# Optimization experiments

Measured on AMD Instinct MI355X. Metric: run time of the kernel, lower is better.

## Reference

```python
import jax, jax.numpy as jnp
import numpy as np

B, H, T, DK = 4, 8, 2048, 64

def setup_inputs() -> dict:
    key = jax.random.key(0)
    kq, kk, kv, kb = jax.random.split(key, 4)
    return {
        "Q": jax.random.normal(kq, (B, H, T, DK), dtype=jnp.float32),
        "K": jax.random.normal(kk, (B, H, T, DK), dtype=jnp.float32),
        "V": jax.random.normal(kv, (B, H, T, DK), dtype=jnp.float32),
        "attn_bias": jax.random.normal(kb, (H, T, T), dtype=jnp.float32),
    }

def reference(Q, K, V, attn_bias):
    # scores = Q K^T / sqrt(d_k) + bias  (bias added post-scaling, as in source)
    d_k = Q.shape[-1]
    scale = 1.0 / jnp.sqrt(jnp.asarray(d_k, Q.dtype))
    scores = jnp.einsum("bhqd,bhkd->bhqk", Q, K) * scale + attn_bias
    attn_weights = jax.nn.softmax(scores, axis=-1)  # (B,H,T,T), rows sum to 1
    # Dropout is identity in eval/reference mode; output uses (pre-dropout) weights.
    output = jnp.einsum("bhqk,bhkd->bhqd", attn_weights, V)
    return (output, attn_weights)
```

## Files before the change

kernel.cpp:

```cpp
#include <hip/hip_runtime.h>
#include <hip/hip_bf16.h>

#define TT   2048
#define DKK  64
#define NHH  8
#define NBB  4
#define QB   128
#define KBLK 64
#define NKT  (TT / KBLK)
#define NJ1  (NKT / 2)
#define LDE  72
#define TILE (KBLK * LDE)
#define SCALE 0.125f

#define SOFT_BARRIER() do {                                         \
    asm volatile("s_waitcnt lgkmcnt(0)" ::: "memory");              \
    __builtin_amdgcn_s_barrier();                                   \
    asm volatile("" ::: "memory");                                  \
} while (0)

typedef __attribute__((ext_vector_type(4))) float  f32x4;
typedef __attribute__((ext_vector_type(8))) __bf16 bf16x8;
typedef __attribute__((ext_vector_type(4))) __bf16 bf16x4;

__global__ __launch_bounds__(256)
void cast_k_kernel(const float* __restrict__ K, __bf16* __restrict__ Kb) {
    size_t i = ((size_t)blockIdx.x * 256 + threadIdx.x) * 8;
    f32x4 a = *(const f32x4*)(K + i);
    f32x4 b = *(const f32x4*)(K + i + 4);
    bf16x8 o = {(__bf16)a[0], (__bf16)a[1], (__bf16)a[2], (__bf16)a[3],
                (__bf16)b[0], (__bf16)b[1], (__bf16)b[2], (__bf16)b[3]};
    *(bf16x8*)(Kb + i) = o;
}

__global__ __launch_bounds__(256)
void vt_kernel(const float* __restrict__ V, __bf16* __restrict__ Vt) {
    __shared__ __bf16 tile[DKK][72];
    const int bh = blockIdx.y;
    const int t0 = blockIdx.x * 64;
    const int tid = threadIdx.x;
    const float* Vb = V + ((size_t)bh * TT + t0) * DKK;
    #pragma unroll
    for (int i = 0; i < 4; ++i) {
        int idx = tid + i * 256;
        int row = idx >> 4, c4 = idx & 15;
        f32x4 v = *(const f32x4*)(Vb + row * DKK + c4 * 4);
        tile[c4 * 4 + 0][row] = (__bf16)v[0];
        tile[c4 * 4 + 1][row] = (__bf16)v[1];
        tile[c4 * 4 + 2][row] = (__bf16)v[2];
        tile[c4 * 4 + 3][row] = (__bf16)v[3];
    }
    __syncthreads();
    __bf16* out = Vt + (size_t)bh * DKK * TT + t0;
    #pragma unroll
    for (int i = 0; i < 2; ++i) {
        int idx = tid + i * 256;
        int d = idx >> 3, ch = idx & 7;
        bf16x8 o = *(const bf16x8*)&tile[d][ch * 8];
        *(bf16x8*)(out + (size_t)d * TT + ch * 8) = o;
    }
}

__global__ __launch_bounds__(512, 4)
void sdpa_main(const float* __restrict__ Qp, const float* __restrict__ Bp,
               const __bf16* __restrict__ Kb, const __bf16* __restrict__ Vt,
               float* __restrict__ Op, float* __restrict__ Wp)
{
    __shared__ __bf16 Bl[4][TILE];
    __shared__ __bf16 Pl[8][16 * LDE];

    const int tid  = threadIdx.x;
    const int lane = tid & 63;
    const int w    = tid >> 6;
    const int g    = lane >> 4;
    const int ql   = lane & 15;

    const int id  = blockIdx.x;
    const int h   = id & 7;
    const int r   = id >> 3;
    const int qt  = r & 15;
    const int b   = r >> 4;
    const int bh  = b * NHH + h;

    const int q_local = w * 16 + ql;
    const int q_glob  = qt * QB + q_local;

    const __bf16* Kbh = Kb + (size_t)bh * TT * DKK;
    const __bf16* Vbh = Vt + (size_t)bh * DKK * TT;
    const float* biasRow = Bp + ((size_t)h * TT + q_glob) * TT;

    const int srow = tid >> 3;
    const int sch  = tid & 7;

    const float* qrow = Qp + ((size_t)bh * TT + q_glob) * DKK;
    f32x4 qa = *(const f32x4*)(qrow + g * 8);
    f32x4 qc = *(const f32x4*)(qrow + g * 8 + 4);
    f32x4 qe = *(const f32x4*)(qrow + 32 + g * 8);
    f32x4 qf = *(const f32x4*)(qrow + 32 + g * 8 + 4);
    const bf16x8 qfrag0 = {(__bf16)qa[0], (__bf16)qa[1], (__bf16)qa[2], (__bf16)qa[3],
                           (__bf16)qc[0], (__bf16)qc[1], (__bf16)qc[2], (__bf16)qc[3]};
    const bf16x8 qfrag1 = {(__bf16)qe[0], (__bf16)qe[1], (__bf16)qe[2], (__bf16)qe[3],
                           (__bf16)qf[0], (__bf16)qf[1], (__bf16)qf[2], (__bf16)qf[3]};

    #pragma unroll
    for (int t = 0; t < 2; ++t) {
        *(bf16x8*)&Bl[t][srow * LDE + sch * 8] =
            *(const bf16x8*)(Kbh + ((size_t)t * KBLK + srow) * DKK + sch * 8);
    }
    __syncthreads();

    f32x4 lacc = {0.f, 0.f, 0.f, 0.f};
    for (int j = 0; j < NJ1; ++j) {
        const int pc = (j & 1) * 2;
        const int pn = ((j + 1) & 1) * 2;
        const bool more = (j + 1 < NJ1);
        bf16x8 kregs[2];
        if (more) {
            #pragma unroll
            for (int t = 0; t < 2; ++t)
                kregs[t] = *(const bf16x8*)(Kbh +
                    ((size_t)((j + 1) * 2 + t) * KBLK + srow) * DKK + sch * 8);
        }
        #pragma unroll
        for (int t = 0; t < 2; ++t) {
            const int kt = j * 2 + t;
            const float* bp = biasRow + kt * KBLK;
            f32x4 bv[4];
            #pragma unroll
            for (int s = 0; s < 4; ++s) bv[s] = *(const f32x4*)(bp + s * 16 + g * 4);
            f32x4 acc[4] = {};
            #pragma unroll
            for (int s = 0; s < 4; ++s) {
                bf16x8 a0 = *(const bf16x8*)&Bl[pc + t][(s * 16 + ql) * LDE + g * 8];
                acc[s] = __builtin_amdgcn_mfma_f32_16x16x32_bf16(a0, qfrag0, acc[s], 0, 0, 0);
                bf16x8 a1 = *(const bf16x8*)&Bl[pc + t][(s * 16 + ql) * LDE + 32 + g * 8];
                acc[s] = __builtin_amdgcn_mfma_f32_16x16x32_bf16(a1, qfrag1, acc[s], 0, 0, 0);
            }
            #pragma unroll
            for (int s = 0; s < 4; ++s) {
                f32x4 x = acc[s] * SCALE + bv[s];
                lacc[0] += __expf(x[0]);
                lacc[1] += __expf(x[1]);
                lacc[2] += __expf(x[2]);
                lacc[3] += __expf(x[3]);
            }
        }
        if (more) {
            #pragma unroll
            for (int t = 0; t < 2; ++t)
                *(bf16x8*)&Bl[pn + t][srow * LDE + sch * 8] = kregs[t];
        }
        SOFT_BARRIER();
    }
    float l_run = lacc[0] + lacc[1] + lacc[2] + lacc[3];
    l_run += __shfl_xor(l_run, 16);
    l_run += __shfl_xor(l_run, 32);
    const float inv_l = 1.0f / l_run;

    __syncthreads();
    *(bf16x8*)&Bl[0][srow * LDE + sch * 8] =
        *(const bf16x8*)(Kbh + (size_t)srow * DKK + sch * 8);
    *(bf16x8*)&Bl[2][srow * LDE + sch * 8] =
        *(const bf16x8*)(Vbh + (size_t)srow * TT + sch * 8);
    __syncthreads();

    f32x4 oacc[4] = {};
    for (int kt = 0; kt < NKT; ++kt) {
        const int cur = kt & 1;
        const bool more = (kt + 1 < NKT);
        bf16x8 kreg, vreg;
        if (more) {
            kreg = *(const bf16x8*)(Kbh + ((size_t)(kt + 1) * KBLK + srow) * DKK + sch * 8);
            vreg = *(const bf16x8*)(Vbh + (size_t)srow * TT + (kt + 1) * KBLK + sch * 8);
        }
        const float* bp = biasRow + kt * KBLK;
        f32x4 bv[4];
        #pragma unroll
        for (int s = 0; s < 4; ++s) bv[s] = *(const f32x4*)(bp + s * 16 + g * 4);

        f32x4 acc[4] = {};
        #pragma unroll
        for (int s = 0; s < 4; ++s) {
            bf16x8 a0 = *(const bf16x8*)&Bl[cur][(s * 16 + ql) * LDE + g * 8];
            acc[s] = __builtin_amdgcn_mfma_f32_16x16x32_bf16(a0, qfrag0, acc[s], 0, 0, 0);
            bf16x8 a1 = *(const bf16x8*)&Bl[cur][(s * 16 + ql) * LDE + 32 + g * 8];
            acc[s] = __builtin_amdgcn_mfma_f32_16x16x32_bf16(a1, qfrag1, acc[s], 0, 0, 0);
        }
        #pragma unroll
        for (int s = 0; s < 4; ++s) {
            f32x4 x = acc[s] * SCALE + bv[s];
            bf16x4 pb = {(__bf16)(__expf(x[0]) * inv_l), (__bf16)(__expf(x[1]) * inv_l),
                         (__bf16)(__expf(x[2]) * inv_l), (__bf16)(__expf(x[3]) * inv_l)};
            *(bf16x4*)&Pl[w][ql * LDE + s * 16 + g * 4] = pb;
        }
        const bf16x8 bp0 = *(const bf16x8*)&Pl[w][ql * LDE + g * 8];
        const bf16x8 bp1 = *(const bf16x8*)&Pl[w][ql * LDE + 32 + g * 8];
        #pragma unroll
        for (int m = 0; m < 4; ++m) {
            bf16x8 av0 = *(const bf16x8*)&Bl[2 + cur][(m * 16 + ql) * LDE + g * 8];
            oacc[m] = __builtin_amdgcn_mfma_f32_16x16x32_bf16(av0, bp0, oacc[m], 0, 0, 0);
            bf16x8 av1 = *(const bf16x8*)&Bl[2 + cur][(m * 16 + ql) * LDE + 32 + g * 8];
            oacc[m] = __builtin_amdgcn_mfma_f32_16x16x32_bf16(av1, bp1, oacc[m], 0, 0, 0);
        }
        #pragma unroll
        for (int s2 = 0; s2 < 4; ++s2) {
            const int wr = s2 * 4 + g;
            bf16x4 pw = *(const bf16x4*)&Pl[w][wr * LDE + ql * 4];
            f32x4 ow = {(float)pw[0], (float)pw[1], (float)pw[2], (float)pw[3]};
            __builtin_nontemporal_store(ow,
                (f32x4*)(Wp + ((size_t)bh * TT + qt * QB + w * 16 + wr) * TT
                             + kt * KBLK + ql * 4));
        }
        if (more) {
            *(bf16x8*)&Bl[cur ^ 1][srow * LDE + sch * 8] = kreg;
            *(bf16x8*)&Bl[2 + (cur ^ 1)][srow * LDE + sch * 8] = vreg;
        }
        SOFT_BARRIER();
    }

    float* Orow = Op + ((size_t)bh * TT + q_glob) * DKK;
    #pragma unroll
    for (int m = 0; m < 4; ++m)
        __builtin_nontemporal_store(oacc[m], (f32x4*)(Orow + m * 16 + g * 4));
}

extern "C" void kernel_launch(void* const* d_in, const int* in_sizes, int n_in,
                              void* d_out, int out_size, void* d_ws, size_t ws_size,
                              hipStream_t stream) {
    const float* Q  = (const float*)d_in[0];
    const float* K  = (const float*)d_in[1];
    const float* V  = (const float*)d_in[2];
    const float* Bs = (const float*)d_in[3];
    float* Out = (float*)d_out;
    float* W   = Out + (size_t)NBB * NHH * TT * DKK;

    const size_t nElem = (size_t)NBB * NHH * TT * DKK;
    __bf16* Kb = (__bf16*)d_ws;
    __bf16* Vt = Kb + nElem;

    cast_k_kernel<<<dim3(nElem / 8 / 256), dim3(256), 0, stream>>>(K, Kb);
    vt_kernel<<<dim3(TT / 64, NBB * NHH), dim3(256), 0, stream>>>(V, Vt);
    sdpa_main<<<dim3((TT / QB) * NBB * NHH), dim3(512), 0, stream>>>(Q, Bs, Kb, Vt, Out, W);
}
```

Measured before the change: 202.4 us.

## Pre-swizzle K into MFMA fragment layout and load directly in pass one

Adds a preprocessing kernel that writes K as bf16 already arranged in per-lane MFMA fragment order. The first pass, which accumulates softmax denominators, then loads fragments straight from global memory into registers. This removes the LDS staging, double buffering and per-iteration barriers from that pass. In exchange it costs an extra pre-kernel launch, extra workspace, and redundant global/L2 reads of K by every wave.

```diff
diff --git a/kernel.cpp b/kernel.cpp
--- a/kernel.cpp
+++ b/kernel.cpp
@@ -31,6 +31,24 @@
     bf16x8 o = {(__bf16)a[0], (__bf16)a[1], (__bf16)a[2], (__bf16)a[3],
                 (__bf16)b[0], (__bf16)b[1], (__bf16)b[2], (__bf16)b[3]};
     *(bf16x8*)(Kb + i) = o;
+}
+
+__global__ __launch_bounds__(512)
+void kf_kernel(const float* __restrict__ K, __bf16* __restrict__ Kf) {
+    const int bh  = blockIdx.y;
+    const int kt  = blockIdx.x;
+    const int tid = threadIdx.x;
+    const int s    = tid >> 7;
+    const int hh   = (tid >> 6) & 1;
+    const int lane = tid & 63;
+    const int ql = lane & 15, g = lane >> 4;
+    const float* src = K + ((size_t)bh * TT + kt * KBLK + s * 16 + ql) * DKK
+                         + hh * 32 + g * 8;
+    f32x4 x = *(const f32x4*)(src);
+    f32x4 y = *(const f32x4*)(src + 4);
+    bf16x8 o = {(__bf16)x[0], (__bf16)x[1], (__bf16)x[2], (__bf16)x[3],
+                (__bf16)y[0], (__bf16)y[1], (__bf16)y[2], (__bf16)y[3]};
+    *(bf16x8*)(Kf + ((size_t)(bh * NKT + kt) * 4096) + (size_t)tid * 8) = o;
 }
 
 __global__ __launch_bounds__(256)
@@ -64,6 +82,7 @@
 __global__ __launch_bounds__(512, 4)
 void sdpa_main(const float* __restrict__ Qp, const float* __restrict__ Bp,
                const __bf16* __restrict__ Kb, const __bf16* __restrict__ Vt,
+               const __bf16* __restrict__ Kf,
                float* __restrict__ Op, float* __restrict__ Wp)
 {
     __shared__ __bf16 Bl[4][TILE];
@@ -87,6 +106,7 @@
 
     const __bf16* Kbh = Kb + (size_t)bh * TT * DKK;
     const __bf16* Vbh = Vt + (size_t)bh * DKK * TT;
+    const __bf16* Kfb = Kf + (size_t)bh * NKT * 4096;
     const float* biasRow = Bp + ((size_t)h * TT + q_glob) * TT;
 
     const int srow = tid >> 3;
@@ -102,28 +122,16 @@
     const bf16x8 qfrag1 = {(__bf16)qe[0], (__bf16)qe[1], (__bf16)qe[2], (__bf16)qe[3],
                            (__bf16)qf[0], (__bf16)qf[1], (__bf16)qf[2], (__bf16)qf[3]};
 
-    #pragma unroll
-    for (int t = 0; t < 2; ++t) {
-        *(bf16x8*)&Bl[t][srow * LDE + sch * 8] =
-            *(const bf16x8*)(Kbh + ((size_t)t * KBLK + srow) * DKK + sch * 8);
-    }
-    __syncthreads();
-
     f32x4 lacc = {0.f, 0.f, 0.f, 0.f};
     for (int j = 0; j < NJ1; ++j) {
-        const int pc = (j & 1) * 2;
-        const int pn = ((j + 1) & 1) * 2;
-        const bool more = (j + 1 < NJ1);
-        bf16x8 kregs[2];
-        if (more) {
-            #pragma unroll
-            for (int t = 0; t < 2; ++t)
-                kregs[t] = *(const bf16x8*)(Kbh +
-                    ((size_t)((j + 1) * 2 + t) * KBLK + srow) * DKK + sch * 8);
-        }
         #pragma unroll
         for (int t = 0; t < 2; ++t) {
             const int kt = j * 2 + t;
+            const __bf16* kf = Kfb + (size_t)kt * 4096 + lane * 8;
+            bf16x8 a[8];
+            #pragma unroll
+            for (int f = 0; f < 8; ++f)
+                a[f] = *(const bf16x8*)(kf + f * 512);
             const float* bp = biasRow + kt * KBLK;
             f32x4 bv[4];
             #pragma unroll
@@ -131,10 +139,8 @@
             f32x4 acc[4] = {};
             #pragma unroll
             for (int s = 0; s < 4; ++s) {
-                bf16x8 a0 = *(const bf16x8*)&Bl[pc + t][(s * 16 + ql) * LDE + g * 8];
-                acc[s] = __builtin_amdgcn_mfma_f32_16x16x32_bf16(a0, qfrag0, acc[s], 0, 0, 0);
-                bf16x8 a1 = *(const bf16x8*)&Bl[pc + t][(s * 16 + ql) * LDE + 32 + g * 8];
-                acc[s] = __builtin_amdgcn_mfma_f32_16x16x32_bf16(a1, qfrag1, acc[s], 0, 0, 0);
+                acc[s] = __builtin_amdgcn_mfma_f32_16x16x32_bf16(a[s * 2],     qfrag0, acc[s], 0, 0, 0);
+                acc[s] = __builtin_amdgcn_mfma_f32_16x16x32_bf16(a[s * 2 + 1], qfrag1, acc[s], 0, 0, 0);
             }
             #pragma unroll
             for (int s = 0; s < 4; ++s) {
@@ -145,19 +151,12 @@
                 lacc[3] += __expf(x[3]);
             }
         }
-        if (more) {
-            #pragma unroll
-            for (int t = 0; t < 2; ++t)
-                *(bf16x8*)&Bl[pn + t][srow * LDE + sch * 8] = kregs[t];
-        }
-        SOFT_BARRIER();
     }
     float l_run = lacc[0] + lacc[1] + lacc[2] + lacc[3];
     l_run += __shfl_xor(l_run, 16);
     l_run += __shfl_xor(l_run, 32);
     const float inv_l = 1.0f / l_run;
 
-    __syncthreads();
     *(bf16x8*)&Bl[0][srow * LDE + sch * 8] =
         *(const bf16x8*)(Kbh + (size_t)srow * DKK + sch * 8);
     *(bf16x8*)&Bl[2][srow * LDE + sch * 8] =
@@ -237,8 +236,10 @@
     const size_t nElem = (size_t)NBB * NHH * TT * DKK;
     __bf16* Kb = (__bf16*)d_ws;
     __bf16* Vt = Kb + nElem;
+    __bf16* Kf = Vt + nElem;
 
     cast_k_kernel<<<dim3(nElem / 8 / 256), dim3(256), 0, stream>>>(K, Kb);
+    kf_kernel<<<dim3(NKT, NBB * NHH), dim3(512), 0, stream>>>(K, Kf);
     vt_kernel<<<dim3(TT / 64, NBB * NHH), dim3(256), 0, stream>>>(V, Vt);
-    sdpa_main<<<dim3((TT / QB) * NBB * NHH), dim3(512), 0, stream>>>(Q, Bs, Kb, Vt, Out, W);
-}
+    sdpa_main<<<dim3((TT / QB) * NBB * NHH), dim3(512), 0, stream>>>(Q, Bs, Kb, Vt, Kf, Out, W);
+}
```

Measured after the change: 226.8 us. 1.12x slower.
